# Optimization experiments

Measured on AMD Instinct MI355X. Metric: run time of the kernel, lower is better.

Reference implementation:

```python
import jax, jax.numpy as jnp
import numpy as np

N, E, D, H = 50000, 1600000, 256, 256
EPS = 1e-5

def prelu(x, a):
    return jnp.where(x >= 0, x, a * x)

def batch_norm(x, gamma, beta):
    # training-mode BatchNorm1d: stats over the node (batch) dim
    mu = jnp.mean(x, axis=0)
    var = jnp.var(x, axis=0)
    return (x - mu) * jax.lax.rsqrt(var + EPS) * gamma + beta

def gcn_conv(x, edge_index, W, b):
    # PyG GCNConv: h = XW, add self-loops, symmetric norm, scatter-add, + bias
    h = x @ W
    n = x.shape[0]
    row = jnp.concatenate([edge_index[0], jnp.arange(n)])
    col = jnp.concatenate([edge_index[1], jnp.arange(n)])
    w = jnp.ones(row.shape[0], dtype=x.dtype)
    deg = jax.ops.segment_sum(w, col, num_segments=n)
    dinv = jnp.where(deg > 0, jax.lax.rsqrt(deg), 0.0)
    norm = dinv[row] * w * dinv[col]  # [E+N]
    msg = h[row] * norm[:, None]      # [E+N, H] gathered messages
    out = jax.ops.segment_sum(msg, col, num_segments=n)
    return out + b

def setup_inputs() -> dict:
    key = jax.random.key(0)
    ks = jax.random.split(key, 10)
    x = jax.random.normal(ks[0], (N, D), dtype=jnp.float32)
    edge_index = jax.random.randint(ks[1], (2, E), 0, N).astype(jnp.int64)
    s1 = 1.0 / np.sqrt(D)
    s2 = 1.0 / np.sqrt(H)
    return {
        "x": x,
        "edge_index": edge_index,
        "W1": jax.random.uniform(ks[2], (D, H), jnp.float32, -s1, s1),
        "b1": jnp.zeros((H,), jnp.float32),
        "W2": jax.random.uniform(ks[3], (H, H), jnp.float32, -s2, s2),
        "b2": jnp.zeros((H,), jnp.float32),
        "prelu_a": jnp.asarray(0.25, jnp.float32),
        "bn_gamma": jnp.ones((H,), jnp.float32),
        "bn_beta": jnp.zeros((H,), jnp.float32),
        "proj_W": jax.random.uniform(ks[4], (H, H), jnp.float32, -s2, s2),
        "proj_b": jnp.zeros((H,), jnp.float32),
        "pbn_gamma": jnp.ones((H,), jnp.float32),
        "pbn_beta": jnp.zeros((H,), jnp.float32),
        "prelu2_a": jnp.asarray(0.25, jnp.float32),
    }

def reference(x, edge_index, W1, b1, W2, b2, prelu_a, bn_gamma, bn_beta,
              proj_W, proj_b, pbn_gamma, pbn_beta, prelu2_a):
    # eval-mode dropout (identity); BN uses batch stats
    z = prelu(gcn_conv(x, edge_index, W1, b1), prelu_a)
    z = prelu(gcn_conv(z, edge_index, W2, b2), prelu_a)
    z = batch_norm(z, bn_gamma, bn_beta)
    p = prelu(batch_norm(z @ proj_W + proj_b, pbn_gamma, pbn_beta), prelu2_a)
    return (z, p)
```

## Files before the change

### kernel.cpp

```cpp
#include <hip/hip_runtime.h>
#include <hip/hip_bf16.h>


#define CAP 96
#define NPB 64
#define CHUNK 2048
#define SEGBIG 2432
#define MAXBKT 1024
#define SEGSTR 16

typedef __attribute__((ext_vector_type(8))) short short8;
typedef __attribute__((ext_vector_type(4))) float f32x4;

__device__ __forceinline__ float bf2f(unsigned short u) {
    union { unsigned int i; float f; } v; v.i = ((unsigned int)u) << 16; return v.f;
}
__device__ __forceinline__ unsigned short f2bf(float f) {
    __hip_bfloat16 h = __float2bfloat16(f);
    return *reinterpret_cast<unsigned short*>(&h);
}

__global__ __launch_bounds__(256) void k_zero(int* segcnt, int nbkt, float* stats) {
    int i = blockIdx.x * 256 + threadIdx.x;
    if (i < nbkt * SEGSTR) segcnt[i] = 0;
    if (i < 2048) stats[i] = 0.0f;
}

__global__ __launch_bounds__(64) void k_zrow(unsigned short* hs, int N) {
    ((ushort4*)hs)[(size_t)N * 64 + threadIdx.x] = ushort4{0, 0, 0, 0};
}

__global__ __launch_bounds__(256) void k_binh(const int* __restrict__ row, const int* __restrict__ col,
                                              unsigned* __restrict__ bins, int* __restrict__ segcnt,
                                              int E, int nbkt) {
    __shared__ int hist[MAXBKT];
    __shared__ int base[MAXBKT];
    int e0 = blockIdx.x * CHUNK;
    int eend = e0 + CHUNK; if (eend > E) eend = E;
    for (int b = threadIdx.x; b < nbkt; b += 256) hist[b] = 0;
    __syncthreads();
    for (int e = e0 + threadIdx.x; e < eend; e += 256)
        atomicAdd(&hist[col[e] >> 6], 1);
    __syncthreads();
    for (int b = threadIdx.x; b < nbkt; b += 256) {
        int h = hist[b];
        base[b] = h ? atomicAdd(&segcnt[b * SEGSTR], h) : 0;
        hist[b] = 0;
    }
    __syncthreads();
    for (int e = e0 + threadIdx.x; e < eend; e += 256) {
        int v = col[e], r = row[e];
        int b = v >> 6;
        int p = base[b] + atomicAdd(&hist[b], 1);
        if (p < SEGBIG) bins[(size_t)b * SEGBIG + p] = ((unsigned)r << 6) | (unsigned)(v & (NPB - 1));
    }
}

__global__ __launch_bounds__(256) void k_csr(const unsigned* __restrict__ bins, const int* __restrict__ segcnt,
                                             int* __restrict__ csr, int* __restrict__ fillp,
                                             float* __restrict__ dinv, int N) {
    __shared__ int cnt[NPB];
    int bkt = blockIdx.x;
    if (threadIdx.x < NPB) cnt[threadIdx.x] = 0;
    __syncthreads();
    int m = segcnt[bkt * SEGSTR]; if (m > SEGBIG) m = SEGBIG;
    const unsigned* b = bins + (size_t)bkt * SEGBIG;
    for (int i = threadIdx.x; i < m; i += 256) {
        unsigned ent = b[i];
        int loc = (int)(ent & (NPB - 1));
        int r   = (int)(ent >> 6);
        int p = atomicAdd(&cnt[loc], 1);
        if (p < CAP) csr[(size_t)(bkt * NPB + loc) * CAP + p] = r;
    }
    __syncthreads();
    if (threadIdx.x < NPB) {
        int v = bkt * NPB + threadIdx.x;
        if (v < N) {
            int c = cnt[threadIdx.x];
            int real = c < CAP ? c : CAP;
            int pc = (real + 15) & ~15;
            if (pc > CAP) pc = CAP;
            int* lst = csr + (size_t)v * CAP;
            for (int p = real; p < pc; ++p) lst[p] = N;
            fillp[v] = pc;
            dinv[v] = rsqrtf(1.0f + (float)c);
        }
    }
}

__global__ __launch_bounds__(256) void k_castx(const float* __restrict__ x, unsigned short* __restrict__ xb, size_t n4) {
    size_t stride = (size_t)gridDim.x * blockDim.x;
    for (size_t i = (size_t)blockIdx.x * blockDim.x + threadIdx.x; i < n4; i += stride) {
        float4 v = ((const float4*)x)[i];
        ushort4 o; o.x = f2bf(v.x); o.y = f2bf(v.y); o.z = f2bf(v.z); o.w = f2bf(v.w);
        ((ushort4*)xb)[i] = o;
    }
}

__global__ __launch_bounds__(256) void k_wt(const float* __restrict__ W, unsigned short* __restrict__ Wt,
                                            const float* __restrict__ scp) {
    __shared__ float t[32][33];
    int bx = blockIdx.x * 32, by = blockIdx.y * 32;
    int x = threadIdx.x & 31, y = threadIdx.x >> 5;
#pragma unroll
    for (int i = 0; i < 32; i += 8) {
        float s = scp ? scp[by + y + i] : 1.0f;
        t[y + i][x] = W[(size_t)(by + y + i) * 256 + bx + x] * s;
    }
    __syncthreads();
#pragma unroll
    for (int i = 0; i < 32; i += 8)
        Wt[(size_t)(bx + y + i) * 256 + by + x] = f2bf(t[x][y + i]);
}

__global__ __launch_bounds__(256) void k_tvec(const float* __restrict__ W, const float* __restrict__ sh,
                                              float* __restrict__ tvec) {
    int n = threadIdx.x;
    float s = 0.0f;
    for (int k = 0; k < 256; ++k) s += sh[k] * W[(size_t)k * 256 + n];
    tvec[n] = s;
}

__global__ __launch_bounds__(256) void k_gemm_bf16(const unsigned short* __restrict__ A,
                                                   const unsigned short* __restrict__ Bt,
                                                   unsigned short* __restrict__ C,
                                                   const float* __restrict__ dinv, int use_scale,
                                                   const float* __restrict__ tvec, int use_bias,
                                                   int M) {
    __shared__ unsigned short buf[16384];
    unsigned short* As = buf;
    unsigned short* Bs = buf + 8192;
    int tid  = threadIdx.x;
    int lane = tid & 63, wid = tid >> 6;
    int wr = wid >> 1, wc = wid & 1;
    int row0 = blockIdx.x * 128;
    int col0 = blockIdx.y * 128;

    f32x4 acc[4][4];
#pragma unroll
    for (int m = 0; m < 4; ++m)
#pragma unroll
        for (int n = 0; n < 4; ++n) acc[m][n] = f32x4{0.f, 0.f, 0.f, 0.f};

    int srow = lane >> 3;
    int sk   = (lane & 7) * 8;

    for (int k0 = 0; k0 < 256; k0 += 64) {
#pragma unroll
        for (int i = 0; i < 4; ++i) {
            int u = i * 4 + wid;
            int arow = row0 + u * 8 + srow;
            if (arow >= M) arow = M - 1;
            const unsigned short* ga = A  + (size_t)arow * 256 + k0 + sk;
            const unsigned short* gb = Bt + (size_t)(col0 + u * 8 + srow) * 256 + k0 + sk;
            __builtin_amdgcn_global_load_lds((const __attribute__((address_space(1))) void*)ga,
                (__attribute__((address_space(3))) void*)(As + u * 512), 16, 0, 0);
            __builtin_amdgcn_global_load_lds((const __attribute__((address_space(1))) void*)gb,
                (__attribute__((address_space(3))) void*)(Bs + u * 512), 16, 0, 0);
        }
        __syncthreads();
#pragma unroll
        for (int kk = 0; kk < 64; kk += 32) {
            short8 a[4], b[4];
#pragma unroll
            for (int m = 0; m < 4; ++m)
                a[m] = *(const short8*)(As + (wr * 64 + m * 16 + (lane & 15)) * 64 + kk + (lane >> 4) * 8);
#pragma unroll
            for (int n = 0; n < 4; ++n)
                b[n] = *(const short8*)(Bs + (wc * 64 + n * 16 + (lane & 15)) * 64 + kk + (lane >> 4) * 8);
#pragma unroll
            for (int m = 0; m < 4; ++m)
#pragma unroll
                for (int n = 0; n < 4; ++n)
                    acc[m][n] = __builtin_amdgcn_mfma_f32_16x16x32_bf16(a[m], b[n], acc[m][n], 0, 0, 0);
        }
        __syncthreads();
    }

    float tn[4] = {0.f, 0.f, 0.f, 0.f};
    if (use_bias) {
#pragma unroll
        for (int n = 0; n < 4; ++n) tn[n] = tvec[col0 + wc * 64 + n * 16 + (lane & 15)];
    }
#pragma unroll
    for (int m = 0; m < 4; ++m)
#pragma unroll
        for (int r = 0; r < 4; ++r) {
            int lr = wr * 64 + m * 16 + (lane >> 4) * 4 + r;
#pragma unroll
            for (int n = 0; n < 4; ++n)
                buf[lr * 128 + wc * 64 + n * 16 + (lane & 15)] = f2bf(acc[m][n][r] + tn[n]);
        }
    __syncthreads();
#pragma unroll
    for (int j = 0; j < 8; ++j) {
        int c = j * 256 + tid;
        int r = c >> 4, cc = c & 15;
        int grow = row0 + r;
        if (grow < M) {
            short8 v = *(const short8*)(buf + r * 128 + cc * 8);
            if (use_scale) {
                float d = dinv[grow];
                short8 o;
#pragma unroll
                for (int t = 0; t < 8; ++t)
                    o[t] = (short)f2bf(bf2f((unsigned short)v[t]) * d);
                v = o;
            }
            *(short8*)(C + (size_t)grow * 256 + col0 + cc * 8) = v;
        }
    }
}

__global__ __launch_bounds__(256) void k_agg_bf(const unsigned short* __restrict__ hs,
                                                unsigned short* __restrict__ outb,
                                                const float* __restrict__ dinv, const int* __restrict__ csr,
                                                const int* __restrict__ fillp, const float* __restrict__ bias,
                                                const float* __restrict__ aptr, int N) {
    int wv = threadIdx.x >> 6, lane = threadIdx.x & 63;
    int v = blockIdx.x * 4 + wv;
    if (v >= N) return;
    const ushort4* h4 = (const ushort4*)hs;
    float dv = dinv[v];
    ushort4 hv = h4[(size_t)v * 64 + lane];
    float s0 = bf2f(hv.x), s1 = bf2f(hv.y), s2 = bf2f(hv.z), s3 = bf2f(hv.w);
    int n = fillp[v];
    const int* lst = csr + (size_t)v * CAP;
    for (int i = 0; i < n; i += 16) {
        int u[16];
        ushort4 a[16];
#pragma unroll
        for (int t = 0; t < 16; ++t) u[t] = lst[i + t];
#pragma unroll
        for (int t = 0; t < 16; ++t) a[t] = h4[(size_t)u[t] * 64 + lane];
#pragma unroll
        for (int t = 0; t < 16; ++t) {
            s0 += bf2f(a[t].x); s1 += bf2f(a[t].y);
            s2 += bf2f(a[t].z); s3 += bf2f(a[t].w);
        }
    }
    float al = *aptr;
    float4 bb = *(const float4*)(bias + lane * 4);
    float o0 = dv * s0 + bb.x, o1 = dv * s1 + bb.y, o2 = dv * s2 + bb.z, o3 = dv * s3 + bb.w;
    o0 = o0 >= 0.f ? o0 : al * o0;
    o1 = o1 >= 0.f ? o1 : al * o1;
    o2 = o2 >= 0.f ? o2 : al * o2;
    o3 = o3 >= 0.f ? o3 : al * o3;
    ushort4 o; o.x = f2bf(o0); o.y = f2bf(o1); o.z = f2bf(o2); o.w = f2bf(o3);
    ((ushort4*)outb)[(size_t)v * 64 + lane] = o;
}

__global__ __launch_bounds__(256) void k_bnstats_v(const unsigned short* __restrict__ X, float* __restrict__ sums, int N) {
    int w = threadIdx.x >> 6, lane = threadIdx.x & 63;
    int c4 = lane * 4;
    float4 s = {0.f, 0.f, 0.f, 0.f}, q = {0.f, 0.f, 0.f, 0.f};
    int rstride = gridDim.x * 4;
    for (int r = blockIdx.x * 4 + w; r < N; r += rstride) {
        ushort4 x4 = ((const ushort4*)X)[(size_t)r * 64 + lane];
        float a = bf2f(x4.x), b = bf2f(x4.y), c = bf2f(x4.z), d = bf2f(x4.w);
        s.x += a; s.y += b; s.z += c; s.w += d;
        q.x += a * a; q.y += b * b; q.z += c * c; q.w += d * d;
    }
    atomicAdd(&sums[c4 + 0], s.x); atomicAdd(&sums[c4 + 1], s.y);
    atomicAdd(&sums[c4 + 2], s.z); atomicAdd(&sums[c4 + 3], s.w);
    atomicAdd(&sums[256 + c4 + 0], q.x); atomicAdd(&sums[256 + c4 + 1], q.y);
    atomicAdd(&sums[256 + c4 + 2], q.z); atomicAdd(&sums[256 + c4 + 3], q.w);
}

__global__ __launch_bounds__(256) void k_bnfinal(float* stats, const float* __restrict__ gamma,
                                                 const float* __restrict__ beta, float invN) {
    int c = threadIdx.x;
    float mu = stats[c] * invN;
    float var = stats[256 + c] * invN - mu * mu;
    float rstd = rsqrtf(var + 1e-5f);
    float sc = rstd * gamma[c];
    stats[512 + c] = sc;
    stats[768 + c] = beta[c] - mu * sc;
}

__global__ __launch_bounds__(256) void k_bnapply_z(const unsigned short* __restrict__ in,
                                                   float* __restrict__ zout,
                                                   const float* __restrict__ scale, const float* __restrict__ shift,
                                                   size_t n4) {
    size_t stride = (size_t)gridDim.x * blockDim.x;
    for (size_t i = (size_t)blockIdx.x * blockDim.x + threadIdx.x; i < n4; i += stride) {
        int c4 = (int)(i & 63) * 4;
        ushort4 x4 = ((const ushort4*)in)[i];
        float4 sc = *(const float4*)(scale + c4);
        float4 sh = *(const float4*)(shift + c4);
        float4 y;
        y.x = bf2f(x4.x) * sc.x + sh.x;
        y.y = bf2f(x4.y) * sc.y + sh.y;
        y.z = bf2f(x4.z) * sc.z + sh.z;
        y.w = bf2f(x4.w) * sc.w + sh.w;
        ((float4*)zout)[i] = y;
    }
}

__global__ __launch_bounds__(256) void k_bnapply_p(const unsigned short* __restrict__ in,
                                                   float* __restrict__ pout,
                                                   const float* __restrict__ scale, const float* __restrict__ shift,
                                                   const float* __restrict__ aptr, size_t n4) {
    size_t stride = (size_t)gridDim.x * blockDim.x;
    float a = *aptr;
    for (size_t i = (size_t)blockIdx.x * blockDim.x + threadIdx.x; i < n4; i += stride) {
        int c4 = (int)(i & 63) * 4;
        ushort4 x4 = ((const ushort4*)in)[i];
        float4 sc = *(const float4*)(scale + c4);
        float4 sh = *(const float4*)(shift + c4);
        float4 y;
        y.x = bf2f(x4.x) * sc.x + sh.x;
        y.y = bf2f(x4.y) * sc.y + sh.y;
        y.z = bf2f(x4.z) * sc.z + sh.z;
        y.w = bf2f(x4.w) * sc.w + sh.w;
        y.x = y.x >= 0.f ? y.x : a * y.x;
        y.y = y.y >= 0.f ? y.y : a * y.y;
        y.z = y.z >= 0.f ? y.z : a * y.z;
        y.w = y.w >= 0.f ? y.w : a * y.w;
        ((float4*)pout)[i] = y;
    }
}

extern "C" void kernel_launch(void* const* d_in, const int* in_sizes, int n_in,
                              void* d_out, int out_size, void* d_ws, size_t ws_size,
                              hipStream_t stream) {
    const float* x     = (const float*)d_in[0];
    const int*   ei    = (const int*)d_in[1];
    const float* W1    = (const float*)d_in[2];
    const float* b1    = (const float*)d_in[3];
    const float* W2    = (const float*)d_in[4];
    const float* b2    = (const float*)d_in[5];
    const float* aptr  = (const float*)d_in[6];
    const float* gamma = (const float*)d_in[7];
    const float* beta  = (const float*)d_in[8];
    const float* projW = (const float*)d_in[9];
    const float* pgamma = (const float*)d_in[11];
    const float* pbeta  = (const float*)d_in[12];
    const float* a2ptr  = (const float*)d_in[13];

    int N = in_sizes[0] / 256;
    int E = in_sizes[1] / 2;
    const int* row = ei;
    const int* col = ei + E;

    float* out  = (float*)d_out;
    float* zout = out;
    float* pout = out + (size_t)N * 256;

    int nbkt = (N + NPB - 1) / NPB;

    size_t rowsz = (size_t)(N + 1) * 256;
    unsigned short* B0 = (unsigned short*)d_ws;
    unsigned short* B1 = B0 + rowsz;
    unsigned short* B2 = B1 + rowsz;
    unsigned short* Wt = B2 + rowsz;
    float* dinv  = (float*)(Wt + 3 * 65536);
    int*   fillp = (int*)(dinv + N + 1);
    int*   csr   = fillp + N;
    float* stats = (float*)(csr + (size_t)N * CAP);
    float* tvec  = stats + 2048;
    int*   segcnt= (int*)(tvec + 256);
    unsigned* bins = (unsigned*)(segcnt + (size_t)nbkt * SEGSTR);

    int nb_binh = (E + CHUNK - 1) / CHUNK;
    dim3 ggrid((N + 127) / 128, 2);
    dim3 wgrid(8, 8);
    int  agrid = (N + 3) / 4;
    size_t n4 = (size_t)N * 64;

    k_zero <<<64, 256, 0, stream>>>(segcnt, nbkt, stats);
    k_zrow <<<1, 64, 0, stream>>>(B1, N);
    k_binh <<<nb_binh, 256, 0, stream>>>(row, col, bins, segcnt, E, nbkt);
    k_csr  <<<nbkt, 256, 0, stream>>>(bins, segcnt, csr, fillp, dinv, N);
    k_castx<<<2048, 256, 0, stream>>>(x, B0, n4);
    k_wt   <<<wgrid, 256, 0, stream>>>(W1, Wt,         nullptr);
    k_wt   <<<wgrid, 256, 0, stream>>>(W2, Wt + 65536, nullptr);

    k_gemm_bf16<<<ggrid, 256, 0, stream>>>(B0, Wt, B1, dinv, 1, nullptr, 0, N);
    k_agg_bf   <<<agrid, 256, 0, stream>>>(B1, B2, dinv, csr, fillp, b1, aptr, N);
    k_gemm_bf16<<<ggrid, 256, 0, stream>>>(B2, Wt + 65536, B1, dinv, 1, nullptr, 0, N);
    k_agg_bf   <<<agrid, 256, 0, stream>>>(B1, B0, dinv, csr, fillp, b2, aptr, N);
    k_bnstats_v<<<128, 256, 0, stream>>>(B0, stats, N);
    k_bnfinal  <<<1, 256, 0, stream>>>(stats, gamma, beta, 1.0f / (float)N);
    k_wt   <<<wgrid, 256, 0, stream>>>(projW, Wt + 131072, stats + 512);
    k_tvec <<<1, 256, 0, stream>>>(projW, stats + 768, tvec);
    k_gemm_bf16<<<ggrid, 256, 0, stream>>>(B0, Wt + 131072, B1, dinv, 0, tvec, 1, N);
    k_bnapply_z<<<2048, 256, 0, stream>>>(B0, zout, stats + 512, stats + 768, n4);
    k_bnstats_v<<<128, 256, 0, stream>>>(B1, stats + 1024, N);
    k_bnfinal  <<<1, 256, 0, stream>>>(stats + 1024, pgamma, pbeta, 1.0f / (float)N);
    k_bnapply_p<<<2048, 256, 0, stream>>>(B1, pout, stats + 1536, stats + 1792, a2ptr, n4);
}
```

Before: 721.8 us.

## Fuse setup, BN-finalize and z-normalization kernels; enlarge edge bucket size

Merges the x cast, weight transposes, zeroing and pad-row init into one setup kernel. BN finalize is folded into the projection-weight prep and the p-apply kernel, and the z normalization is written from the projection GEMM's A tiles instead of a separate pass. Edge binning moves to 128 nodes per bucket with larger chunks. The aim is fewer launches and one less full read of the activations. The cost is z writes with an 8-float per-thread stride inside the GEMM and recomputing BN scales in every block.

```diff
diff --git a/kernel.cpp b/kernel.cpp
--- a/kernel.cpp
+++ b/kernel.cpp
@@ -3,11 +3,12 @@
 
 
 #define CAP 96
-#define NPB 64
-#define CHUNK 2048
-#define SEGBIG 2432
-#define MAXBKT 1024
+#define NPB 128
+#define CHUNK 4096
+#define SEGBIG 4608
+#define MAXBKT 512
 #define SEGSTR 16
+#define BNEPS 1e-5f
 
 typedef __attribute__((ext_vector_type(8))) short short8;
 typedef __attribute__((ext_vector_type(4))) float f32x4;
@@ -20,14 +21,41 @@
     return *reinterpret_cast<unsigned short*>(&h);
 }
 
-__global__ __launch_bounds__(256) void k_zero(int* segcnt, int nbkt, float* stats) {
-    int i = blockIdx.x * 256 + threadIdx.x;
-    if (i < nbkt * SEGSTR) segcnt[i] = 0;
-    if (i < 2048) stats[i] = 0.0f;
-}
-
-__global__ __launch_bounds__(64) void k_zrow(unsigned short* hs, int N) {
-    ((ushort4*)hs)[(size_t)N * 64 + threadIdx.x] = ushort4{0, 0, 0, 0};
+__global__ __launch_bounds__(256) void k_setup(const float* __restrict__ x, unsigned short* __restrict__ xb,
+                                               const float* __restrict__ W1, unsigned short* __restrict__ Wt1,
+                                               const float* __restrict__ W2, unsigned short* __restrict__ Wt2,
+                                               int* segcnt, int nbkt, float* stats,
+                                               unsigned short* zrowbuf, int N, size_t n4) {
+    int bid = blockIdx.x;
+    if (bid < 1024) {
+        size_t stride = (size_t)1024 * 256;
+        for (size_t i = (size_t)bid * 256 + threadIdx.x; i < n4; i += stride) {
+            float4 v = ((const float4*)x)[i];
+            ushort4 o; o.x = f2bf(v.x); o.y = f2bf(v.y); o.z = f2bf(v.z); o.w = f2bf(v.w);
+            ((ushort4*)xb)[i] = o;
+        }
+    } else if (bid < 1152) {
+        const float* W = bid < 1088 ? W1 : W2;
+        unsigned short* Wt = bid < 1088 ? Wt1 : Wt2;
+        int widx = (bid - 1024) & 63;
+        int bx = (widx & 7) * 32, by = (widx >> 3) * 32;
+        __shared__ float t[32][33];
+        int xx = threadIdx.x & 31, yy = threadIdx.x >> 5;
+#pragma unroll
+        for (int i = 0; i < 32; i += 8)
+            t[yy + i][xx] = W[(size_t)(by + yy + i) * 256 + bx + xx];
+        __syncthreads();
+#pragma unroll
+        for (int i = 0; i < 32; i += 8)
+            Wt[(size_t)(bx + yy + i) * 256 + by + xx] = f2bf(t[xx][yy + i]);
+    } else if (bid < 1184) {
+        int i = (bid - 1152) * 256 + threadIdx.x;
+        if (i < nbkt * SEGSTR) segcnt[i] = 0;
+        if (i < 2048) stats[i] = 0.0f;
+    } else {
+        if (threadIdx.x < 64)
+            ((ushort4*)zrowbuf)[(size_t)N * 64 + threadIdx.x] = ushort4{0, 0, 0, 0};
+    }
 }
 
 __global__ __launch_bounds__(256) void k_binh(const int* __restrict__ row, const int* __restrict__ col,
@@ -40,7 +68,7 @@
     for (int b = threadIdx.x; b < nbkt; b += 256) hist[b] = 0;
     __syncthreads();
     for (int e = e0 + threadIdx.x; e < eend; e += 256)
-        atomicAdd(&hist[col[e] >> 6], 1);
+        atomicAdd(&hist[col[e] >> 7], 1);
     __syncthreads();
     for (int b = threadIdx.x; b < nbkt; b += 256) {
         int h = hist[b];
@@ -50,9 +78,9 @@
     __syncthreads();
     for (int e = e0 + threadIdx.x; e < eend; e += 256) {
         int v = col[e], r = row[e];
-        int b = v >> 6;
+        int b = v >> 7;
         int p = base[b] + atomicAdd(&hist[b], 1);
-        if (p < SEGBIG) bins[(size_t)b * SEGBIG + p] = ((unsigned)r << 6) | (unsigned)(v & (NPB - 1));
+        if (p < SEGBIG) bins[(size_t)b * SEGBIG + p] = ((unsigned)r << 7) | (unsigned)(v & (NPB - 1));
     }
 }
 
@@ -68,7 +96,7 @@
     for (int i = threadIdx.x; i < m; i += 256) {
         unsigned ent = b[i];
         int loc = (int)(ent & (NPB - 1));
-        int r   = (int)(ent >> 6);
+        int r   = (int)(ent >> 7);
         int p = atomicAdd(&cnt[loc], 1);
         if (p < CAP) csr[(size_t)(bkt * NPB + loc) * CAP + p] = r;
     }
@@ -88,37 +116,39 @@
     }
 }
 
-__global__ __launch_bounds__(256) void k_castx(const float* __restrict__ x, unsigned short* __restrict__ xb, size_t n4) {
-    size_t stride = (size_t)gridDim.x * blockDim.x;
-    for (size_t i = (size_t)blockIdx.x * blockDim.x + threadIdx.x; i < n4; i += stride) {
-        float4 v = ((const float4*)x)[i];
-        ushort4 o; o.x = f2bf(v.x); o.y = f2bf(v.y); o.z = f2bf(v.z); o.w = f2bf(v.w);
-        ((ushort4*)xb)[i] = o;
-    }
-}
-
-__global__ __launch_bounds__(256) void k_wt(const float* __restrict__ W, unsigned short* __restrict__ Wt,
-                                            const float* __restrict__ scp) {
-    __shared__ float t[32][33];
-    int bx = blockIdx.x * 32, by = blockIdx.y * 32;
-    int x = threadIdx.x & 31, y = threadIdx.x >> 5;
-#pragma unroll
-    for (int i = 0; i < 32; i += 8) {
-        float s = scp ? scp[by + y + i] : 1.0f;
-        t[y + i][x] = W[(size_t)(by + y + i) * 256 + bx + x] * s;
-    }
-    __syncthreads();
-#pragma unroll
-    for (int i = 0; i < 32; i += 8)
-        Wt[(size_t)(bx + y + i) * 256 + by + x] = f2bf(t[x][y + i]);
-}
-
-__global__ __launch_bounds__(256) void k_tvec(const float* __restrict__ W, const float* __restrict__ sh,
-                                              float* __restrict__ tvec) {
-    int n = threadIdx.x;
-    float s = 0.0f;
-    for (int k = 0; k < 256; ++k) s += sh[k] * W[(size_t)k * 256 + n];
-    tvec[n] = s;
+__global__ __launch_bounds__(256) void k_wtb(const float* __restrict__ W, unsigned short* __restrict__ Wt,
+                                             const float* __restrict__ sums,
+                                             const float* __restrict__ gamma, const float* __restrict__ beta,
+                                             float invN, float* __restrict__ tvec) {
+    int bid = blockIdx.x;
+    if (bid < 64) {
+        int bx = (bid & 7) * 32, by = (bid >> 3) * 32;
+        __shared__ float t[32][33];
+        int xx = threadIdx.x & 31, yy = threadIdx.x >> 5;
+#pragma unroll
+        for (int i = 0; i < 32; i += 8) {
+            int k = by + yy + i;
+            float mu = sums[k] * invN;
+            float var = sums[256 + k] * invN - mu * mu;
+            float sc = rsqrtf(var + BNEPS) * gamma[k];
+            t[yy + i][xx] = W[(size_t)k * 256 + bx + xx] * sc;
+        }
+        __syncthreads();
+#pragma unroll
+        for (int i = 0; i < 32; i += 8)
+            Wt[(size_t)(bx + yy + i) * 256 + by + xx] = f2bf(t[xx][yy + i]);
+    } else {
+        int n = threadIdx.x;
+        float s = 0.0f;
+        for (int k = 0; k < 256; ++k) {
+            float mu = sums[k] * invN;
+            float var = sums[256 + k] * invN - mu * mu;
+            float sc = rsqrtf(var + BNEPS) * gamma[k];
+            float sh = beta[k] - mu * sc;
+            s += sh * W[(size_t)k * 256 + n];
+        }
+        tvec[n] = s;
+    }
 }
 
 __global__ __launch_bounds__(256) void k_gemm_bf16(const unsigned short* __restrict__ A,
@@ -126,8 +156,12 @@
                                                    unsigned short* __restrict__ C,
                                                    const float* __restrict__ dinv, int use_scale,
                                                    const float* __restrict__ tvec, int use_bias,
+                                                   const float* __restrict__ bnsums,
+                                                   const float* __restrict__ gamma, const float* __restrict__ beta,
+                                                   float invN, float* __restrict__ zout, int writez,
                                                    int M) {
     __shared__ unsigned short buf[16384];
+    __shared__ float zsc[256], zsh[256];
     unsigned short* As = buf;
     unsigned short* Bs = buf + 8192;
     int tid  = threadIdx.x;
@@ -135,6 +169,14 @@
     int wr = wid >> 1, wc = wid & 1;
     int row0 = blockIdx.x * 128;
     int col0 = blockIdx.y * 128;
+
+    if (writez) {
+        int c = tid;
+        float mu = bnsums[c] * invN;
+        float var = bnsums[256 + c] * invN - mu * mu;
+        float sc = rsqrtf(var + BNEPS) * gamma[c];
+        zsc[c] = sc; zsh[c] = beta[c] - mu * sc;
+    }
 
     f32x4 acc[4][4];
 #pragma unroll
@@ -159,6 +201,21 @@
                 (__attribute__((address_space(3))) void*)(Bs + u * 512), 16, 0, 0);
         }
         __syncthreads();
+        if (writez && blockIdx.y == 0) {
+#pragma unroll
+            for (int j = 0; j < 4; ++j) {
+                int r = j * 32 + (tid >> 3);
+                int kk = (tid & 7) * 8;
+                int grow = row0 + r;
+                if (grow < M) {
+                    short8 v = *(const short8*)(As + (r >> 3) * 512 + (r & 7) * 64 + kk);
+                    float* zp = zout + (size_t)grow * 256 + k0 + kk;
+#pragma unroll
+                    for (int t = 0; t < 8; ++t)
+                        zp[t] = bf2f((unsigned short)v[t]) * zsc[k0 + kk + t] + zsh[k0 + kk + t];
+                }
+            }
+        }
 #pragma unroll
         for (int kk = 0; kk < 64; kk += 32) {
             short8 a[4], b[4];
@@ -267,52 +324,30 @@
     atomicAdd(&sums[256 + c4 + 2], q.z); atomicAdd(&sums[256 + c4 + 3], q.w);
 }
 
-__global__ __launch_bounds__(256) void k_bnfinal(float* stats, const float* __restrict__ gamma,
-                                                 const float* __restrict__ beta, float invN) {
-    int c = threadIdx.x;
-    float mu = stats[c] * invN;
-    float var = stats[256 + c] * invN - mu * mu;
-    float rstd = rsqrtf(var + 1e-5f);
-    float sc = rstd * gamma[c];
-    stats[512 + c] = sc;
-    stats[768 + c] = beta[c] - mu * sc;
-}
-
-__global__ __launch_bounds__(256) void k_bnapply_z(const unsigned short* __restrict__ in,
-                                                   float* __restrict__ zout,
-                                                   const float* __restrict__ scale, const float* __restrict__ shift,
-                                                   size_t n4) {
-    size_t stride = (size_t)gridDim.x * blockDim.x;
-    for (size_t i = (size_t)blockIdx.x * blockDim.x + threadIdx.x; i < n4; i += stride) {
-        int c4 = (int)(i & 63) * 4;
-        ushort4 x4 = ((const ushort4*)in)[i];
-        float4 sc = *(const float4*)(scale + c4);
-        float4 sh = *(const float4*)(shift + c4);
-        float4 y;
-        y.x = bf2f(x4.x) * sc.x + sh.x;
-        y.y = bf2f(x4.y) * sc.y + sh.y;
-        y.z = bf2f(x4.z) * sc.z + sh.z;
-        y.w = bf2f(x4.w) * sc.w + sh.w;
-        ((float4*)zout)[i] = y;
-    }
-}
-
-__global__ __launch_bounds__(256) void k_bnapply_p(const unsigned short* __restrict__ in,
-                                                   float* __restrict__ pout,
-                                                   const float* __restrict__ scale, const float* __restrict__ shift,
-                                                   const float* __restrict__ aptr, size_t n4) {
+__global__ __launch_bounds__(256) void k_bnp(const unsigned short* __restrict__ in,
+                                             float* __restrict__ pout,
+                                             const float* __restrict__ sums,
+                                             const float* __restrict__ gamma, const float* __restrict__ beta,
+                                             float invN, const float* __restrict__ aptr, size_t n4) {
+    __shared__ float psc[256], psh[256];
+    {
+        int c = threadIdx.x;
+        float mu = sums[c] * invN;
+        float var = sums[256 + c] * invN - mu * mu;
+        float sc = rsqrtf(var + BNEPS) * gamma[c];
+        psc[c] = sc; psh[c] = beta[c] - mu * sc;
+    }
+    __syncthreads();
     size_t stride = (size_t)gridDim.x * blockDim.x;
     float a = *aptr;
     for (size_t i = (size_t)blockIdx.x * blockDim.x + threadIdx.x; i < n4; i += stride) {
         int c4 = (int)(i & 63) * 4;
         ushort4 x4 = ((const ushort4*)in)[i];
-        float4 sc = *(const float4*)(scale + c4);
-        float4 sh = *(const float4*)(shift + c4);
         float4 y;
-        y.x = bf2f(x4.x) * sc.x + sh.x;
-        y.y = bf2f(x4.y) * sc.y + sh.y;
-        y.z = bf2f(x4.z) * sc.z + sh.z;
-        y.w = bf2f(x4.w) * sc.w + sh.w;
+        y.x = bf2f(x4.x) * psc[c4 + 0] + psh[c4 + 0];
+        y.y = bf2f(x4.y) * psc[c4 + 1] + psh[c4 + 1];
+        y.z = bf2f(x4.z) * psc[c4 + 2] + psh[c4 + 2];
+        y.w = bf2f(x4.w) * psc[c4 + 3] + psh[c4 + 3];
         y.x = y.x >= 0.f ? y.x : a * y.x;
         y.y = y.y >= 0.f ? y.y : a * y.y;
         y.z = y.z >= 0.f ? y.z : a * y.z;
@@ -348,6 +383,7 @@
     float* pout = out + (size_t)N * 256;
 
     int nbkt = (N + NPB - 1) / NPB;
+    float invN = 1.0f / (float)N;
 
     size_t rowsz = (size_t)(N + 1) * 256;
     unsigned short* B0 = (unsigned short*)d_ws;
@@ -364,29 +400,23 @@
 
     int nb_binh = (E + CHUNK - 1) / CHUNK;
     dim3 ggrid((N + 127) / 128, 2);
-    dim3 wgrid(8, 8);
     int  agrid = (N + 3) / 4;
     size_t n4 = (size_t)N * 64;
 
-    k_zero <<<64, 256, 0, stream>>>(segcnt, nbkt, stats);
-    k_zrow <<<1, 64, 0, stream>>>(B1, N);
+    k_setup<<<1185, 256, 0, stream>>>(x, B0, W1, Wt, W2, Wt + 65536,
+                                      segcnt, nbkt, stats, B1, N, n4);
     k_binh <<<nb_binh, 256, 0, stream>>>(row, col, bins, segcnt, E, nbkt);
     k_csr  <<<nbkt, 256, 0, stream>>>(bins, segcnt, csr, fillp, dinv, N);
-    k_castx<<<2048, 256, 0, stream>>>(x, B0, n4);
-    k_wt   <<<wgrid, 256, 0, stream>>>(W1, Wt,         nullptr);
-    k_wt   <<<wgrid, 256, 0, stream>>>(W2, Wt + 65536, nullptr);
-
-    k_gemm_bf16<<<ggrid, 256, 0, stream>>>(B0, Wt, B1, dinv, 1, nullptr, 0, N);
+    k_gemm_bf16<<<ggrid, 256, 0, stream>>>(B0, Wt, B1, dinv, 1, nullptr, 0,
+                                           nullptr, nullptr, nullptr, 0.f, nullptr, 0, N);
     k_agg_bf   <<<agrid, 256, 0, stream>>>(B1, B2, dinv, csr, fillp, b1, aptr, N);
-    k_gemm_bf16<<<ggrid, 256, 0, stream>>>(B2, Wt + 65536, B1, dinv, 1, nullptr, 0, N);
+    k_gemm_bf16<<<ggrid, 256, 0, stream>>>(B2, Wt + 65536, B1, dinv, 1, nullptr, 0,
+                                           nullptr, nullptr, nullptr, 0.f, nullptr, 0, N);
     k_agg_bf   <<<agrid, 256, 0, stream>>>(B1, B0, dinv, csr, fillp, b2, aptr, N);
     k_bnstats_v<<<128, 256, 0, stream>>>(B0, stats, N);
-    k_bnfinal  <<<1, 256, 0, stream>>>(stats, gamma, beta, 1.0f / (float)N);
-    k_wt   <<<wgrid, 256, 0, stream>>>(projW, Wt + 131072, stats + 512);
-    k_tvec <<<1, 256, 0, stream>>>(projW, stats + 768, tvec);
-    k_gemm_bf16<<<ggrid, 256, 0, stream>>>(B0, Wt + 131072, B1, dinv, 0, tvec, 1, N);
-    k_bnapply_z<<<2048, 256, 0, stream>>>(B0, zout, stats + 512, stats + 768, n4);
+    k_wtb<<<65, 256, 0, stream>>>(projW, Wt + 131072, stats, gamma, beta, invN, tvec);
+    k_gemm_bf16<<<ggrid, 256, 0, stream>>>(B0, Wt + 131072, B1, dinv, 0, tvec, 1,
+                                           stats, gamma, beta, invN, zout, 1, N);
     k_bnstats_v<<<128, 256, 0, stream>>>(B1, stats + 1024, N);
-    k_bnfinal  <<<1, 256, 0, stream>>>(stats + 1024, pgamma, pbeta, 1.0f / (float)N);
-    k_bnapply_p<<<2048, 256, 0, stream>>>(B1, pout, stats + 1536, stats + 1792, a2ptr, n4);
-}
+    k_bnp<<<2048, 256, 0, stream>>>(B1, pout, stats + 1024, pgamma, pbeta, invN, a2ptr, n4);
+}
```

After: 681.7 us. -5.5%, faster.
